# Optimization experiments

Hardware: AMD Instinct MI355X
Metric: run time of the kernel (lower is better)

The kernel has to match this reference:

```python
import jax, jax.numpy as jnp
import numpy as np

USER_NUM = 300000
ITEM_NUM = 200000
EMBED_DIM = 64
N_EDGES = 1250000
N_LAYERS = 3  # len([embedding_dim] + hidden_units) with hidden_units=[64,64]
N_NODES = USER_NUM + ITEM_NUM


def setup_inputs() -> dict:
    key = jax.random.key(0)
    k1, k2, k3, k4, k5 = jax.random.split(key, 5)
    user_emb = 0.01 * jax.random.normal(k1, (USER_NUM, EMBED_DIM), dtype=jnp.float32)
    item_emb = 0.01 * jax.random.normal(k2, (ITEM_NUM, EMBED_DIM), dtype=jnp.float32)
    edge_weight = jax.random.uniform(k3, (N_EDGES,), dtype=jnp.float32)
    src_idx = jax.random.randint(k4, (N_EDGES,), 0, N_NODES, dtype=jnp.int32)
    dst_idx = jax.random.randint(k5, (N_EDGES,), 0, N_NODES, dtype=jnp.int32)
    return {"user_emb": user_emb, "item_emb": item_emb, "edge_weight": edge_weight,
            "src_idx": src_idx, "dst_idx": dst_idx}


def reference(user_emb, item_emb, edge_weight, src_idx, dst_idx):
    # computer(): concat embeddings -> L hops of sparse.mm(adj, emb) -> mean over hops -> split
    all_emb = jnp.concatenate([user_emb, item_emb], axis=0)  # [N, d]
    acc = all_emb  # running sum of per-hop embeddings (includes hop 0)
    h = all_emb
    for _ in range(N_LAYERS):
        # weighted SpMM: out[dst] += w * h[src]
        msgs = h[src_idx] * edge_weight[:, None]            # [E, d]
        h = jax.ops.segment_sum(msgs, dst_idx, num_segments=N_NODES)  # [N, d]
        acc = acc + h
    light_out = acc / jnp.float32(N_LAYERS + 1)             # mean over stacked hops
    return light_out[:USER_NUM], light_out[USER_NUM:]
```

## Files before the change

### kernel.cpp

```cpp
#include <hip/hip_runtime.h>


#define USER_NUM  300000
#define ITEM_NUM  200000
#define N_NODES   500000
#define EMBED_DIM 64
#define N_EDGES   1250000
#define NV   (N_NODES * EMBED_DIM)
#define NV4  (NV / 4)

#define BSHIFT  11
#define BNODES  2048
#define NBUK    ((N_NODES + BNODES - 1) / BNODES)
#define PCHUNK  4096
#define PGRID   ((N_EDGES + PCHUNK - 1) / PCHUNK)

__device__ __forceinline__ unsigned bpack(float lo, float hi) {
    unsigned a = __float_as_uint(lo), b = __float_as_uint(hi);
    a = (a + 0x7fffu + ((a >> 16) & 1u)) >> 16;
    b = (b + 0x7fffu + ((b >> 16) & 1u)) & 0xffff0000u;
    return a | b;
}
__device__ __forceinline__ float blo(unsigned u) { return __uint_as_float(u << 16); }
__device__ __forceinline__ float bhi(unsigned u) { return __uint_as_float(u & 0xffff0000u); }

__device__ __forceinline__ void bf8_fma(uint4 g, float w, float* a) {
    a[0] += w * blo(g.x); a[1] += w * bhi(g.x);
    a[2] += w * blo(g.y); a[3] += w * bhi(g.y);
    a[4] += w * blo(g.z); a[5] += w * bhi(g.z);
    a[6] += w * blo(g.w); a[7] += w * bhi(g.w);
}

__global__ void bhist_kernel(const int* __restrict__ dst, int* __restrict__ bcnt) {
    __shared__ int h[256];
    int t = threadIdx.x;
    h[t] = 0;
    __syncthreads();
    int cbase = blockIdx.x * PCHUNK;
    int cnt = min(PCHUNK, N_EDGES - cbase);
    for (int i = t; i < cnt; i += 256)
        atomicAdd(&h[dst[cbase + i] >> BSHIFT], 1);
    __syncthreads();
    if (t < NBUK && h[t]) atomicAdd(&bcnt[t], h[t]);
}

__global__ void bscan_kernel(const int* __restrict__ bcnt,
                             int* __restrict__ boff,
                             int* __restrict__ bcur,
                             int* __restrict__ offs) {
    __shared__ int lds[256];
    int t = threadIdx.x;
    int v = (t < NBUK) ? bcnt[t] : 0;
    lds[t] = v;
    __syncthreads();
    for (int off = 1; off < 256; off <<= 1) {
        int x = (t >= off) ? lds[t - off] : 0;
        __syncthreads();
        if (t >= off) lds[t] += x;
        __syncthreads();
    }
    int excl = lds[t] - v;
    if (t < NBUK) { boff[t] = excl; bcur[t] = excl; }
    if (t == NBUK - 1) boff[NBUK] = N_EDGES;
    if (t == 0) offs[N_NODES] = N_EDGES;
}

__global__ void part_kernel(const int* __restrict__ src,
                            const int* __restrict__ dst,
                            const float* __restrict__ w,
                            int* __restrict__ bcur,
                            int4* __restrict__ tmp) {
    __shared__ int hist[256];
    __shared__ int base[256];
    int t = threadIdx.x;
    int cbase = blockIdx.x * PCHUNK;
    int cnt = min(PCHUNK, N_EDGES - cbase);
    int es[16], ed[16];
    float ew[16];
    hist[t] = 0;
    __syncthreads();
    #pragma unroll
    for (int k = 0; k < 16; ++k) {
        int i = t + k * 256;
        if (i < cnt) {
            int e = cbase + i;
            es[k] = src[e]; ed[k] = dst[e]; ew[k] = w[e];
            atomicAdd(&hist[ed[k] >> BSHIFT], 1);
        } else ed[k] = -1;
    }
    __syncthreads();
    int h = hist[t];
    base[t] = (h > 0) ? atomicAdd(&bcur[t], h) : 0;
    __syncthreads();
    hist[t] = 0;
    __syncthreads();
    #pragma unroll
    for (int k = 0; k < 16; ++k) {
        if (ed[k] >= 0) {
            int b = ed[k] >> BSHIFT;
            int r = atomicAdd(&hist[b], 1);
            tmp[base[b] + r] = make_int4(es[k], __float_as_int(ew[k]), ed[k], 0);
        }
    }
}

__global__ void fine_kernel(const int4* __restrict__ tmp,
                            const int* __restrict__ boff,
                            int* __restrict__ offs,
                            int2* __restrict__ pe) {
    __shared__ int cnt[BNODES];
    __shared__ int sums[256];
    int b = blockIdx.x, t = threadIdx.x;
    int nbase = b << BSHIFT;
    int ebeg = boff[b], eend = boff[b + 1];
    for (int j = t; j < BNODES; j += 256) cnt[j] = 0;
    __syncthreads();
    for (int i = ebeg + t; i < eend; i += 256)
        atomicAdd(&cnt[tmp[i].z - nbase], 1);
    __syncthreads();
    int s[8], tot = 0;
    #pragma unroll
    for (int k = 0; k < 8; ++k) { s[k] = cnt[t * 8 + k]; tot += s[k]; }
    sums[t] = tot;
    __syncthreads();
    for (int off = 1; off < 256; off <<= 1) {
        int x = (t >= off) ? sums[t - off] : 0;
        __syncthreads();
        if (t >= off) sums[t] += x;
        __syncthreads();
    }
    int run = ebeg + sums[t] - tot;
    #pragma unroll
    for (int k = 0; k < 8; ++k) {
        int node = nbase + t * 8 + k;
        if (node < N_NODES) offs[node] = run;
        cnt[t * 8 + k] = run;
        run += s[k];
    }
    __syncthreads();
    for (int i = ebeg + t; i < eend; i += 256) {
        int4 E = tmp[i];
        int p = atomicAdd(&cnt[E.z - nbase], 1);
        pe[p] = make_int2(E.x, E.y);
    }
}

__global__ void layer1_kernel(const float4* __restrict__ ue,
                              const float4* __restrict__ ie,
                              uint4* __restrict__ hout,
                              const int* __restrict__ offs,
                              const int2* __restrict__ pe) {
    int gid  = blockIdx.x * blockDim.x + threadIdx.x;
    int wave = gid >> 6;
    int lane = gid & 63;
    int grp  = lane >> 3;
    int sub  = lane & 7;
    int n    = wave * 8 + grp;
    if (n >= N_NODES) return;
    int beg = offs[n], end = offs[n + 1];
    float a0[8] = {0,0,0,0,0,0,0,0};
    float a1[8] = {0,0,0,0,0,0,0,0};
    int e = beg;
    for (; e + 2 <= end; e += 2) {
        int2 p0 = pe[e], p1 = pe[e + 1];
        const float4* s0p = (p0.x < USER_NUM) ? &ue[(size_t)p0.x * 16]
                                              : &ie[(size_t)(p0.x - USER_NUM) * 16];
        const float4* s1p = (p1.x < USER_NUM) ? &ue[(size_t)p1.x * 16]
                                              : &ie[(size_t)(p1.x - USER_NUM) * 16];
        float4 g0a = s0p[sub * 2], g0b = s0p[sub * 2 + 1];
        float4 g1a = s1p[sub * 2], g1b = s1p[sub * 2 + 1];
        float w0 = __int_as_float(p0.y), w1 = __int_as_float(p1.y);
        a0[0] += w0 * g0a.x; a0[1] += w0 * g0a.y; a0[2] += w0 * g0a.z; a0[3] += w0 * g0a.w;
        a0[4] += w0 * g0b.x; a0[5] += w0 * g0b.y; a0[6] += w0 * g0b.z; a0[7] += w0 * g0b.w;
        a1[0] += w1 * g1a.x; a1[1] += w1 * g1a.y; a1[2] += w1 * g1a.z; a1[3] += w1 * g1a.w;
        a1[4] += w1 * g1b.x; a1[5] += w1 * g1b.y; a1[6] += w1 * g1b.z; a1[7] += w1 * g1b.w;
    }
    if (e < end) {
        int2 p0 = pe[e];
        const float4* s0p = (p0.x < USER_NUM) ? &ue[(size_t)p0.x * 16]
                                              : &ie[(size_t)(p0.x - USER_NUM) * 16];
        float4 g0a = s0p[sub * 2], g0b = s0p[sub * 2 + 1];
        float w0 = __int_as_float(p0.y);
        a0[0] += w0 * g0a.x; a0[1] += w0 * g0a.y; a0[2] += w0 * g0a.z; a0[3] += w0 * g0a.w;
        a0[4] += w0 * g0b.x; a0[5] += w0 * g0b.y; a0[6] += w0 * g0b.z; a0[7] += w0 * g0b.w;
    }
    #pragma unroll
    for (int i = 0; i < 8; ++i) a0[i] += a1[i];
    uint4 r;
    r.x = bpack(a0[0], a0[1]); r.y = bpack(a0[2], a0[3]);
    r.z = bpack(a0[4], a0[5]); r.w = bpack(a0[6], a0[7]);
    hout[(size_t)n * 8 + sub] = r;
}

__global__ void layer2_kernel(const uint4* __restrict__ hsrc,
                              uint4* __restrict__ hout,
                              const int* __restrict__ offs,
                              const int2* __restrict__ pe) {
    int gid  = blockIdx.x * blockDim.x + threadIdx.x;
    int wave = gid >> 6;
    int lane = gid & 63;
    int grp  = lane >> 3;
    int sub  = lane & 7;
    int n    = wave * 8 + grp;
    if (n >= N_NODES) return;
    int beg = offs[n], end = offs[n + 1];
    float a0[8] = {0,0,0,0,0,0,0,0};
    float a1[8] = {0,0,0,0,0,0,0,0};
    int e = beg;
    for (; e + 2 <= end; e += 2) {
        int2 p0 = pe[e], p1 = pe[e + 1];
        uint4 g0 = hsrc[(size_t)p0.x * 8 + sub];
        uint4 g1 = hsrc[(size_t)p1.x * 8 + sub];
        bf8_fma(g0, __int_as_float(p0.y), a0);
        bf8_fma(g1, __int_as_float(p1.y), a1);
    }
    if (e < end) {
        int2 p0 = pe[e];
        uint4 g0 = hsrc[(size_t)p0.x * 8 + sub];
        bf8_fma(g0, __int_as_float(p0.y), a0);
    }
    #pragma unroll
    for (int i = 0; i < 8; ++i) a0[i] += a1[i];
    uint4 r;
    r.x = bpack(a0[0], a0[1]); r.y = bpack(a0[2], a0[3]);
    r.z = bpack(a0[4], a0[5]); r.w = bpack(a0[6], a0[7]);
    hout[(size_t)n * 8 + sub] = r;
}

__global__ void final_kernel(const float4* __restrict__ ue,
                             const float4* __restrict__ ie,
                             const uint4* __restrict__ h1,
                             const uint4* __restrict__ h2,
                             float4* __restrict__ out,
                             const int* __restrict__ offs,
                             const int2* __restrict__ pe) {
    int gid  = blockIdx.x * blockDim.x + threadIdx.x;
    int wave = gid >> 6;
    int lane = gid & 63;
    int grp  = lane >> 3;
    int sub  = lane & 7;
    int n    = wave * 8 + grp;
    if (n >= N_NODES) return;
    int beg = offs[n], end = offs[n + 1];
    float a0[8] = {0,0,0,0,0,0,0,0};
    float a1[8] = {0,0,0,0,0,0,0,0};
    int e = beg;
    for (; e + 2 <= end; e += 2) {
        int2 p0 = pe[e], p1 = pe[e + 1];
        uint4 g0 = h2[(size_t)p0.x * 8 + sub];
        uint4 g1 = h2[(size_t)p1.x * 8 + sub];
        bf8_fma(g0, __int_as_float(p0.y), a0);
        bf8_fma(g1, __int_as_float(p1.y), a1);
    }
    if (e < end) {
        int2 p0 = pe[e];
        uint4 g0 = h2[(size_t)p0.x * 8 + sub];
        bf8_fma(g0, __int_as_float(p0.y), a0);
    }
    size_t o8 = (size_t)n * 8 + sub;
    uint4 b1 = h1[o8], b2 = h2[o8];
    const float4* e0p = (n < USER_NUM) ? &ue[(size_t)n * 16]
                                       : &ie[(size_t)(n - USER_NUM) * 16];
    float4 e0a = e0p[sub * 2], e0b = e0p[sub * 2 + 1];
    float4 ra, rb;
    ra.x = 0.25f * (e0a.x + blo(b1.x) + blo(b2.x) + a0[0] + a1[0]);
    ra.y = 0.25f * (e0a.y + bhi(b1.x) + bhi(b2.x) + a0[1] + a1[1]);
    ra.z = 0.25f * (e0a.z + blo(b1.y) + blo(b2.y) + a0[2] + a1[2]);
    ra.w = 0.25f * (e0a.w + bhi(b1.y) + bhi(b2.y) + a0[3] + a1[3]);
    rb.x = 0.25f * (e0b.x + blo(b1.z) + blo(b2.z) + a0[4] + a1[4]);
    rb.y = 0.25f * (e0b.y + bhi(b1.z) + bhi(b2.z) + a0[5] + a1[5]);
    rb.z = 0.25f * (e0b.z + blo(b1.w) + blo(b2.w) + a0[6] + a1[6]);
    rb.w = 0.25f * (e0b.w + bhi(b1.w) + bhi(b2.w) + a0[7] + a1[7]);
    out[(size_t)n * 16 + sub * 2]     = ra;
    out[(size_t)n * 16 + sub * 2 + 1] = rb;
}

__global__ void init_fb_kernel(const float4* __restrict__ ue,
                               const float4* __restrict__ ie,
                               float4* __restrict__ h,
                               float4* __restrict__ hn,
                               float4* __restrict__ acc) {
    int i = blockIdx.x * blockDim.x + threadIdx.x;
    if (i >= NV4) return;
    const int ub = USER_NUM * EMBED_DIM / 4;
    float4 v = (i < ub) ? ue[i] : ie[i - ub];
    h[i] = v; acc[i] = v;
    hn[i] = make_float4(0.f, 0.f, 0.f, 0.f);
}

__global__ void spmm_fb_kernel(const float* __restrict__ h, float* __restrict__ hn,
                               const int* __restrict__ src, const int* __restrict__ dst,
                               const float* __restrict__ w) {
    int gid = blockIdx.x * blockDim.x + threadIdx.x;
    int wave = gid >> 6, lane = gid & 63;
    int nwave = (gridDim.x * blockDim.x) >> 6;
    for (int e = wave; e < N_EDGES; e += nwave) {
        float v = h[src[e] * 64 + lane] * w[e];
        atomicAdd(&hn[dst[e] * 64 + lane], v);
    }
}

template <int LAST>
__global__ void accum_fb_kernel(float4* __restrict__ acc, const float4* __restrict__ hn,
                                float4* __restrict__ zbuf) {
    int i = blockIdx.x * blockDim.x + threadIdx.x;
    if (i >= NV4) return;
    float4 a = acc[i], n = hn[i];
    a.x += n.x; a.y += n.y; a.z += n.z; a.w += n.w;
    if (LAST) { a.x *= 0.25f; a.y *= 0.25f; a.z *= 0.25f; a.w *= 0.25f; }
    acc[i] = a;
    if (!LAST) zbuf[i] = make_float4(0.f, 0.f, 0.f, 0.f);
}

extern "C" void kernel_launch(void* const* d_in, const int* in_sizes, int n_in,
                              void* d_out, int out_size, void* d_ws, size_t ws_size,
                              hipStream_t stream) {
    const float* ue  = (const float*)d_in[0];
    const float* ie  = (const float*)d_in[1];
    const float* w   = (const float*)d_in[2];
    const int*   src = (const int*)d_in[3];
    const int*   dst = (const int*)d_in[4];

    float* out = (float*)d_out;

    const size_t HB = (size_t)N_NODES * 128;
    char*  base = (char*)d_ws;
    uint4* B    = (uint4*)base;
    uint4* C    = (uint4*)(base + HB);
    int4*  tmp  = (int4*)(base + 2 * HB);
    int2*  pe   = (int2*)(base + 2 * HB + (size_t)N_EDGES * 16);
    int*   offs = (int*)((char*)pe + (size_t)N_EDGES * 8);
    int*   boff = offs + (N_NODES + 1);
    int*   bcnt = boff + (NBUK + 1);
    int*   bcur = bcnt + NBUK;

    const size_t needed = 2 * HB + (size_t)N_EDGES * 24
                        + (size_t)(N_NODES + 1 + 3 * NBUK + 1) * 4;

    const int TB = 256;
    const int egrid = NV4 / TB;
    const int fgrid = (N_NODES / 8 * 64) / TB;

    if (ws_size >= needed) {
        hipMemsetAsync(bcnt, 0, (size_t)NBUK * 4, stream);
        bhist_kernel<<<PGRID, TB, 0, stream>>>(dst, bcnt);
        bscan_kernel<<<1, 256, 0, stream>>>(bcnt, boff, bcur, offs);
        part_kernel<<<PGRID, TB, 0, stream>>>(src, dst, w, bcur, tmp);
        fine_kernel<<<NBUK, TB, 0, stream>>>(tmp, boff, offs, pe);

        layer1_kernel<<<fgrid, TB, 0, stream>>>((const float4*)ue, (const float4*)ie,
                                                B, offs, pe);
        layer2_kernel<<<fgrid, TB, 0, stream>>>(B, C, offs, pe);
        final_kernel<<<fgrid, TB, 0, stream>>>((const float4*)ue, (const float4*)ie,
                                               B, C, (float4*)out, offs, pe);
    } else {
        float* A  = (float*)d_ws;
        float* Bf = A + NV;
        const int sgrid = 4096;
        init_fb_kernel<<<egrid, TB, 0, stream>>>((const float4*)ue, (const float4*)ie,
                                                 (float4*)A, (float4*)Bf, (float4*)out);
        spmm_fb_kernel<<<sgrid, TB, 0, stream>>>(A, Bf, src, dst, w);
        accum_fb_kernel<0><<<egrid, TB, 0, stream>>>((float4*)out, (const float4*)Bf, (float4*)A);
        spmm_fb_kernel<<<sgrid, TB, 0, stream>>>(Bf, A, src, dst, w);
        accum_fb_kernel<0><<<egrid, TB, 0, stream>>>((float4*)out, (const float4*)A, (float4*)Bf);
        spmm_fb_kernel<<<sgrid, TB, 0, stream>>>(A, Bf, src, dst, w);
        accum_fb_kernel<1><<<egrid, TB, 0, stream>>>((float4*)out, (const float4*)Bf, nullptr);
    }
}
```

Measured before the change: 252.2 us.

## Pre-convert embeddings to bf16 and pack partition keys into int2

```diff
diff --git a/kernel.cpp b/kernel.cpp
--- a/kernel.cpp
+++ b/kernel.cpp
@@ -29,6 +29,21 @@
     a[2] += w * blo(g.y); a[3] += w * bhi(g.y);
     a[4] += w * blo(g.z); a[5] += w * bhi(g.z);
     a[6] += w * blo(g.w); a[7] += w * bhi(g.w);
+}
+
+__global__ void conv_kernel(const float4* __restrict__ ue,
+                            const float4* __restrict__ ie,
+                            uint4* __restrict__ E) {
+    int i = blockIdx.x * blockDim.x + threadIdx.x;
+    if (i >= N_NODES * 8) return;
+    int n = i >> 3, sub = i & 7;
+    const float4* p = (n < USER_NUM) ? &ue[(size_t)n * 16]
+                                     : &ie[(size_t)(n - USER_NUM) * 16];
+    float4 a = p[sub * 2], b = p[sub * 2 + 1];
+    uint4 r;
+    r.x = bpack(a.x, a.y); r.y = bpack(a.z, a.w);
+    r.z = bpack(b.x, b.y); r.w = bpack(b.z, b.w);
+    E[i] = r;
 }
 
 __global__ void bhist_kernel(const int* __restrict__ dst, int* __restrict__ bcnt) {
@@ -69,13 +84,13 @@
                             const int* __restrict__ dst,
                             const float* __restrict__ w,
                             int* __restrict__ bcur,
-                            int4* __restrict__ tmp) {
+                            int2* __restrict__ tmp) {
     __shared__ int hist[256];
     __shared__ int base[256];
     int t = threadIdx.x;
     int cbase = blockIdx.x * PCHUNK;
     int cnt = min(PCHUNK, N_EDGES - cbase);
-    int es[16], ed[16];
+    int key[16], eb[16];
     float ew[16];
     hist[t] = 0;
     __syncthreads();
@@ -84,9 +99,12 @@
         int i = t + k * 256;
         if (i < cnt) {
             int e = cbase + i;
-            es[k] = src[e]; ed[k] = dst[e]; ew[k] = w[e];
-            atomicAdd(&hist[ed[k] >> BSHIFT], 1);
-        } else ed[k] = -1;
+            int d = dst[e];
+            eb[k]  = d >> BSHIFT;
+            key[k] = ((d & (BNODES - 1)) << 19) | src[e];
+            ew[k]  = w[e];
+            atomicAdd(&hist[eb[k]], 1);
+        } else eb[k] = -1;
     }
     __syncthreads();
     int h = hist[t];
@@ -96,15 +114,14 @@
     __syncthreads();
     #pragma unroll
     for (int k = 0; k < 16; ++k) {
-        if (ed[k] >= 0) {
-            int b = ed[k] >> BSHIFT;
-            int r = atomicAdd(&hist[b], 1);
-            tmp[base[b] + r] = make_int4(es[k], __float_as_int(ew[k]), ed[k], 0);
+        if (eb[k] >= 0) {
+            int r = atomicAdd(&hist[eb[k]], 1);
+            tmp[base[eb[k]] + r] = make_int2(key[k], __float_as_int(ew[k]));
         }
     }
 }
 
-__global__ void fine_kernel(const int4* __restrict__ tmp,
+__global__ void fine_kernel(const int2* __restrict__ tmp,
                             const int* __restrict__ boff,
                             int* __restrict__ offs,
                             int2* __restrict__ pe) {
@@ -116,7 +133,7 @@
     for (int j = t; j < BNODES; j += 256) cnt[j] = 0;
     __syncthreads();
     for (int i = ebeg + t; i < eend; i += 256)
-        atomicAdd(&cnt[tmp[i].z - nbase], 1);
+        atomicAdd(&cnt[((unsigned)tmp[i].x) >> 19], 1);
     __syncthreads();
     int s[8], tot = 0;
     #pragma unroll
@@ -139,63 +156,16 @@
     }
     __syncthreads();
     for (int i = ebeg + t; i < eend; i += 256) {
-        int4 E = tmp[i];
-        int p = atomicAdd(&cnt[E.z - nbase], 1);
-        pe[p] = make_int2(E.x, E.y);
-    }
-}
-
-__global__ void layer1_kernel(const float4* __restrict__ ue,
-                              const float4* __restrict__ ie,
-                              uint4* __restrict__ hout,
-                              const int* __restrict__ offs,
-                              const int2* __restrict__ pe) {
-    int gid  = blockIdx.x * blockDim.x + threadIdx.x;
-    int wave = gid >> 6;
-    int lane = gid & 63;
-    int grp  = lane >> 3;
-    int sub  = lane & 7;
-    int n    = wave * 8 + grp;
-    if (n >= N_NODES) return;
-    int beg = offs[n], end = offs[n + 1];
-    float a0[8] = {0,0,0,0,0,0,0,0};
-    float a1[8] = {0,0,0,0,0,0,0,0};
-    int e = beg;
-    for (; e + 2 <= end; e += 2) {
-        int2 p0 = pe[e], p1 = pe[e + 1];
-        const float4* s0p = (p0.x < USER_NUM) ? &ue[(size_t)p0.x * 16]
-                                              : &ie[(size_t)(p0.x - USER_NUM) * 16];
-        const float4* s1p = (p1.x < USER_NUM) ? &ue[(size_t)p1.x * 16]
-                                              : &ie[(size_t)(p1.x - USER_NUM) * 16];
-        float4 g0a = s0p[sub * 2], g0b = s0p[sub * 2 + 1];
-        float4 g1a = s1p[sub * 2], g1b = s1p[sub * 2 + 1];
-        float w0 = __int_as_float(p0.y), w1 = __int_as_float(p1.y);
-        a0[0] += w0 * g0a.x; a0[1] += w0 * g0a.y; a0[2] += w0 * g0a.z; a0[3] += w0 * g0a.w;
-        a0[4] += w0 * g0b.x; a0[5] += w0 * g0b.y; a0[6] += w0 * g0b.z; a0[7] += w0 * g0b.w;
-        a1[0] += w1 * g1a.x; a1[1] += w1 * g1a.y; a1[2] += w1 * g1a.z; a1[3] += w1 * g1a.w;
-        a1[4] += w1 * g1b.x; a1[5] += w1 * g1b.y; a1[6] += w1 * g1b.z; a1[7] += w1 * g1b.w;
-    }
-    if (e < end) {
-        int2 p0 = pe[e];
-        const float4* s0p = (p0.x < USER_NUM) ? &ue[(size_t)p0.x * 16]
-                                              : &ie[(size_t)(p0.x - USER_NUM) * 16];
-        float4 g0a = s0p[sub * 2], g0b = s0p[sub * 2 + 1];
-        float w0 = __int_as_float(p0.y);
-        a0[0] += w0 * g0a.x; a0[1] += w0 * g0a.y; a0[2] += w0 * g0a.z; a0[3] += w0 * g0a.w;
-        a0[4] += w0 * g0b.x; a0[5] += w0 * g0b.y; a0[6] += w0 * g0b.z; a0[7] += w0 * g0b.w;
-    }
-    #pragma unroll
-    for (int i = 0; i < 8; ++i) a0[i] += a1[i];
-    uint4 r;
-    r.x = bpack(a0[0], a0[1]); r.y = bpack(a0[2], a0[3]);
-    r.z = bpack(a0[4], a0[5]); r.w = bpack(a0[6], a0[7]);
-    hout[(size_t)n * 8 + sub] = r;
-}
-
-__global__ void layer2_kernel(const uint4* __restrict__ hsrc,
-                              uint4* __restrict__ hout,
-                              const int* __restrict__ offs,
-                              const int2* __restrict__ pe) {
+        int2 E2 = tmp[i];
+        int p = atomicAdd(&cnt[((unsigned)E2.x) >> 19], 1);
+        pe[p] = make_int2(E2.x & 0x7FFFF, E2.y);
+    }
+}
+
+__global__ void layer_kernel(const uint4* __restrict__ hsrc,
+                             uint4* __restrict__ hout,
+                             const int* __restrict__ offs,
+                             const int2* __restrict__ pe) {
     int gid  = blockIdx.x * blockDim.x + threadIdx.x;
     int wave = gid >> 6;
     int lane = gid & 63;
@@ -227,8 +197,7 @@
     hout[(size_t)n * 8 + sub] = r;
 }
 
-__global__ void final_kernel(const float4* __restrict__ ue,
-                             const float4* __restrict__ ie,
+__global__ void final_kernel(const uint4* __restrict__ E,
                              const uint4* __restrict__ h1,
                              const uint4* __restrict__ h2,
                              float4* __restrict__ out,
@@ -258,19 +227,16 @@
         bf8_fma(g0, __int_as_float(p0.y), a0);
     }
     size_t o8 = (size_t)n * 8 + sub;
-    uint4 b1 = h1[o8], b2 = h2[o8];
-    const float4* e0p = (n < USER_NUM) ? &ue[(size_t)n * 16]
-                                       : &ie[(size_t)(n - USER_NUM) * 16];
-    float4 e0a = e0p[sub * 2], e0b = e0p[sub * 2 + 1];
+    uint4 e0 = E[o8], b1 = h1[o8], b2 = h2[o8];
     float4 ra, rb;
-    ra.x = 0.25f * (e0a.x + blo(b1.x) + blo(b2.x) + a0[0] + a1[0]);
-    ra.y = 0.25f * (e0a.y + bhi(b1.x) + bhi(b2.x) + a0[1] + a1[1]);
-    ra.z = 0.25f * (e0a.z + blo(b1.y) + blo(b2.y) + a0[2] + a1[2]);
-    ra.w = 0.25f * (e0a.w + bhi(b1.y) + bhi(b2.y) + a0[3] + a1[3]);
-    rb.x = 0.25f * (e0b.x + blo(b1.z) + blo(b2.z) + a0[4] + a1[4]);
-    rb.y = 0.25f * (e0b.y + bhi(b1.z) + bhi(b2.z) + a0[5] + a1[5]);
-    rb.z = 0.25f * (e0b.z + blo(b1.w) + blo(b2.w) + a0[6] + a1[6]);
-    rb.w = 0.25f * (e0b.w + bhi(b1.w) + bhi(b2.w) + a0[7] + a1[7]);
+    ra.x = 0.25f * (blo(e0.x) + blo(b1.x) + blo(b2.x) + a0[0] + a1[0]);
+    ra.y = 0.25f * (bhi(e0.x) + bhi(b1.x) + bhi(b2.x) + a0[1] + a1[1]);
+    ra.z = 0.25f * (blo(e0.y) + blo(b1.y) + blo(b2.y) + a0[2] + a1[2]);
+    ra.w = 0.25f * (bhi(e0.y) + bhi(b1.y) + bhi(b2.y) + a0[3] + a1[3]);
+    rb.x = 0.25f * (blo(e0.z) + blo(b1.z) + blo(b2.z) + a0[4] + a1[4]);
+    rb.y = 0.25f * (bhi(e0.z) + bhi(b1.z) + bhi(b2.z) + a0[5] + a1[5]);
+    rb.z = 0.25f * (blo(e0.w) + blo(b1.w) + blo(b2.w) + a0[6] + a1[6]);
+    rb.w = 0.25f * (bhi(e0.w) + bhi(b1.w) + bhi(b2.w) + a0[7] + a1[7]);
     out[(size_t)n * 16 + sub * 2]     = ra;
     out[(size_t)n * 16 + sub * 2 + 1] = rb;
 }
@@ -325,20 +291,22 @@
 
     const size_t HB = (size_t)N_NODES * 128;
     char*  base = (char*)d_ws;
-    uint4* B    = (uint4*)base;
-    uint4* C    = (uint4*)(base + HB);
-    int4*  tmp  = (int4*)(base + 2 * HB);
-    int2*  pe   = (int2*)(base + 2 * HB + (size_t)N_EDGES * 16);
+    uint4* E    = (uint4*)base;
+    uint4* B    = (uint4*)(base + HB);
+    uint4* C    = (uint4*)(base + 2 * HB);
+    int2*  tmp  = (int2*)(base + 3 * HB);
+    int2*  pe   = (int2*)(base + 3 * HB + (size_t)N_EDGES * 8);
     int*   offs = (int*)((char*)pe + (size_t)N_EDGES * 8);
     int*   boff = offs + (N_NODES + 1);
     int*   bcnt = boff + (NBUK + 1);
     int*   bcur = bcnt + NBUK;
 
-    const size_t needed = 2 * HB + (size_t)N_EDGES * 24
+    const size_t needed = 3 * HB + (size_t)N_EDGES * 16
                         + (size_t)(N_NODES + 1 + 3 * NBUK + 1) * 4;
 
     const int TB = 256;
     const int egrid = NV4 / TB;
+    const int cgrid = (N_NODES * 8) / TB + 1;
     const int fgrid = (N_NODES / 8 * 64) / TB;
 
     if (ws_size >= needed) {
@@ -347,12 +315,11 @@
         bscan_kernel<<<1, 256, 0, stream>>>(bcnt, boff, bcur, offs);
         part_kernel<<<PGRID, TB, 0, stream>>>(src, dst, w, bcur, tmp);
         fine_kernel<<<NBUK, TB, 0, stream>>>(tmp, boff, offs, pe);
-
-        layer1_kernel<<<fgrid, TB, 0, stream>>>((const float4*)ue, (const float4*)ie,
-                                                B, offs, pe);
-        layer2_kernel<<<fgrid, TB, 0, stream>>>(B, C, offs, pe);
-        final_kernel<<<fgrid, TB, 0, stream>>>((const float4*)ue, (const float4*)ie,
-                                               B, C, (float4*)out, offs, pe);
+        conv_kernel<<<cgrid, TB, 0, stream>>>((const float4*)ue, (const float4*)ie, E);
+
+        layer_kernel<<<fgrid, TB, 0, stream>>>(E, B, offs, pe);
+        layer_kernel<<<fgrid, TB, 0, stream>>>(B, C, offs, pe);
+        final_kernel<<<fgrid, TB, 0, stream>>>(E, B, C, (float4*)out, offs, pe);
     } else {
         float* A  = (float*)d_ws;
         float* Bf = A + NV;
```

Result: no change. 255.6 us (+1.4%).
